# Optimization experiments

Measured on AMD Instinct MI355X. Metric: run time of the kernel, lower is better.

Reference implementation:

```python
import jax, jax.numpy as jnp
import numpy as np

B, T, I, H, O = 64, 512, 256, 512, 1


def _rnn_layer(x, W_ih, W_hh, b_ih, b_hh):
    """One ReLU-RNN layer. x: [B,T,D] -> [B,T,H]."""
    # Precompute input projection for all timesteps as one big GEMM.
    xw = jnp.einsum('btd,hd->bth', x, W_ih) + b_ih + b_hh  # [B,T,H]

    def step(h, xt):
        h = jax.nn.relu(xt + h @ W_hh.T)  # [B,H]
        return h, h

    h0 = jnp.zeros((x.shape[0], W_hh.shape[0]), x.dtype)
    _, out = jax.lax.scan(step, h0, jnp.swapaxes(xw, 0, 1))  # [T,B,H]
    return jnp.swapaxes(out, 0, 1)


def setup_inputs() -> dict:
    key = jax.random.key(0)
    ks = jax.random.split(key, 11)
    s_i = 1.0 / np.sqrt(H)
    inp = {
        'x': jax.random.normal(ks[0], (B, T, I), dtype=jnp.float32),
        'W_ih0': jax.random.uniform(ks[1], (H, I), jnp.float32, -s_i, s_i),
        'W_hh0': jax.random.uniform(ks[2], (H, H), jnp.float32, -s_i, s_i),
        'b_ih0': jax.random.uniform(ks[3], (H,), jnp.float32, -s_i, s_i),
        'b_hh0': jax.random.uniform(ks[4], (H,), jnp.float32, -s_i, s_i),
        'W_ih1': jax.random.uniform(ks[5], (H, H), jnp.float32, -s_i, s_i),
        'W_hh1': jax.random.uniform(ks[6], (H, H), jnp.float32, -s_i, s_i),
        'b_ih1': jax.random.uniform(ks[7], (H,), jnp.float32, -s_i, s_i),
        'b_hh1': jax.random.uniform(ks[8], (H,), jnp.float32, -s_i, s_i),
        'W_fc': jax.random.uniform(ks[9], (O, H), jnp.float32, -s_i, s_i),
        'b_fc': jax.random.uniform(ks[10], (O,), jnp.float32, -s_i, s_i),
    }
    return inp


def reference(x, W_ih0, W_hh0, b_ih0, b_hh0, W_ih1, W_hh1, b_ih1, b_hh1, W_fc, b_fc):
    h = _rnn_layer(x, W_ih0, W_hh0, b_ih0, b_hh0)   # layer 0
    h = _rnn_layer(h, W_ih1, W_hh1, b_ih1, b_hh1)   # layer 1
    logits = jnp.einsum('bth,oh->bto', h, W_fc) + b_fc
    return jax.nn.sigmoid(logits)  # [B,T,O]
```

## Files before the change

### kernel.cpp

```cpp
#include <hip/hip_runtime.h>


typedef _Float16 half8 __attribute__((ext_vector_type(8)));
typedef _Float16 half4 __attribute__((ext_vector_type(4)));
typedef float    f32x4 __attribute__((ext_vector_type(4)));

#define T_DIM 512
#define H_DIM 512
#define B_DIM 64
#define CHUNK 16

#define RAW_BARRIER() asm volatile("s_waitcnt lgkmcnt(0)\n\ts_barrier" ::: "memory")

__global__ __launch_bounds__(256) void conv_w_f16(
    const float* __restrict__ in, _Float16* __restrict__ out)
{
    int i = (blockIdx.x * 256 + threadIdx.x) * 4;
    float4 v = *(const float4*)(in + i);
    out[i + 0] = (_Float16)v.x;
    out[i + 1] = (_Float16)v.y;
    out[i + 2] = (_Float16)v.z;
    out[i + 3] = (_Float16)v.w;
}

__global__ __launch_bounds__(64) void init_flags(int* flags)
{
    flags[threadIdx.x & 31] = 0;
}

__global__ __launch_bounds__(256) void gemm_proj0(
    const float* __restrict__ A32,
    const float* __restrict__ W,
    const float* __restrict__ b1,
    const float* __restrict__ b2,
    _Float16* __restrict__ xwF)
{
    __shared__ float As[16][68];
    __shared__ float Bs[16][68];

    const int tx = threadIdx.x & 15;
    const int ty = threadIdx.x >> 4;
    const int t  = blockIdx.x;
    const int n0 = blockIdx.y * 64;

    float acc[4][4] = {};
    const int rr  = threadIdx.x >> 2;
    const int kk4 = (threadIdx.x & 3) * 4;

    for (int kc = 0; kc < 256; kc += 16) {
        {
            float4 av = *(const float4*)(A32 + (size_t)(rr * T_DIM + t) * 256 + kc + kk4);
            As[kk4 + 0][rr] = av.x; As[kk4 + 1][rr] = av.y;
            As[kk4 + 2][rr] = av.z; As[kk4 + 3][rr] = av.w;
            float4 wv = *(const float4*)(W + (size_t)(n0 + rr) * 256 + kc + kk4);
            Bs[kk4 + 0][rr] = wv.x; Bs[kk4 + 1][rr] = wv.y;
            Bs[kk4 + 2][rr] = wv.z; Bs[kk4 + 3][rr] = wv.w;
        }
        __syncthreads();
#pragma unroll
        for (int kk = 0; kk < 16; ++kk) {
            float4 av = *(const float4*)&As[kk][ty * 4];
            float4 bv = *(const float4*)&Bs[kk][tx * 4];
            float a[4] = {av.x, av.y, av.z, av.w};
            float b[4] = {bv.x, bv.y, bv.z, bv.w};
#pragma unroll
            for (int i = 0; i < 4; ++i)
#pragma unroll
                for (int j = 0; j < 4; ++j)
                    acc[i][j] = fmaf(a[i], b[j], acc[i][j]);
        }
        __syncthreads();
    }

#pragma unroll
    for (int j = 0; j < 4; ++j) {
        int n = n0 + tx * 4 + j;
        float bias = b1[n] + b2[n];
        half4 hv;
#pragma unroll
        for (int i = 0; i < 4; ++i) hv[i] = (_Float16)(acc[i][j] + bias);
        size_t addr = ((size_t)t * 4 + (ty >> 2)) * 8192
                    + ((size_t)blockIdx.y * 4 + (tx >> 2)) * 256
                    + (ty & 3) * 64 + ((tx & 3) * 4 + j) * 4;
        *(half4*)&xwF[addr] = hv;
    }
}

__global__ __launch_bounds__(512, 2) void pipeline(
    const _Float16* __restrict__ xwF0,
    _Float16* __restrict__ xwF1,
    _Float16* __restrict__ h0A,
    const _Float16* __restrict__ W16_0,
    const _Float16* __restrict__ W16_1,
    const float* __restrict__ Wih1,
    const float* __restrict__ bih1,
    const float* __restrict__ bhh1,
    const float* __restrict__ wfc,
    float* __restrict__ part,
    int* __restrict__ flags)
{
    __shared__ _Float16 smem[65536];

    const int bx   = blockIdx.x;
    const int tid  = threadIdx.x;
    const int w    = tid >> 6;
    const int lane = tid & 63;
    const int col  = lane & 15;
    const int q    = lane >> 4;

    int* flag0 = flags;
    int* flag1 = flags + 4;

    if (bx >= 4 && bx < 20) {
        const int g = (bx - 4) >> 2;
        const int s = (bx - 4) & 3;
        _Float16* Bls = smem;

        for (int grp = w; grp < 128; grp += 8) {
            int kt = grp >> 3, nt = grp & 7;
            int n  = s * 128 + nt * 16 + col;
            int k0 = kt * 32 + q * 8;
            float4 a = *(const float4*)(Wih1 + (size_t)n * 512 + k0);
            float4 b = *(const float4*)(Wih1 + (size_t)n * 512 + k0 + 4);
            half8 hv;
            hv[0] = (_Float16)a.x; hv[1] = (_Float16)a.y;
            hv[2] = (_Float16)a.z; hv[3] = (_Float16)a.w;
            hv[4] = (_Float16)b.x; hv[5] = (_Float16)b.y;
            hv[6] = (_Float16)b.z; hv[7] = (_Float16)b.w;
            *(half8*)&Bls[(grp * 64 + lane) * 8] = hv;
        }
        float bias[8];
#pragma unroll
        for (int nt = 0; nt < 8; ++nt) {
            int n = s * 128 + nt * 16 + col;
            bias[nt] = bih1[n] + bhh1[n];
        }
        __syncthreads();

        for (int c = 0; c < T_DIM / CHUNK; ++c) {
            while (__hip_atomic_load(&flag0[g], __ATOMIC_ACQUIRE,
                                     __HIP_MEMORY_SCOPE_AGENT) < c + 1)
                __builtin_amdgcn_s_sleep(2);

#pragma unroll
            for (int i = 0; i < 2; ++i) {
                int t = c * CHUNK + w * 2 + i;
                f32x4 acc[8] = {};
#pragma unroll
                for (int kt = 0; kt < 16; ++kt) {
                    half8 a = *(const half8*)(
                        h0A + ((size_t)(g * T_DIM + t) * 16 + kt) * 512 + lane * 8);
#pragma unroll
                    for (int nt = 0; nt < 8; ++nt) {
                        half8 bfr = *(const half8*)&Bls[((kt * 8 + nt) * 64 + lane) * 8];
                        acc[nt] = __builtin_amdgcn_mfma_f32_16x16x32_f16(
                            a, bfr, acc[nt], 0, 0, 0);
                    }
                }
                _Float16* dst = xwF1 + ((size_t)t * 4 + g) * 8192;
#pragma unroll
                for (int nt = 0; nt < 8; ++nt) {
                    half4 hv;
#pragma unroll
                    for (int r = 0; r < 4; ++r)
                        hv[r] = (_Float16)(acc[nt][r] + bias[nt]);
                    *(half4*)(dst + (s * 8 + nt) * 256 + q * 64 + col * 4) = hv;
                }
            }
            __syncthreads();
            if (tid == 0)
                __hip_atomic_store(&flag1[g * 4 + s], c + 1, __ATOMIC_RELEASE,
                                   __HIP_MEMORY_SCOPE_AGENT);
        }
        return;
    }

    const bool L0 = (bx < 4);
    const int  g  = L0 ? bx : bx - 20;
    const _Float16* W16 = L0 ? W16_0 : W16_1;
    const _Float16* xwF = L0 ? xwF0 : xwF1;

    _Float16* WlB = smem;
    _Float16* hA  = smem + 49152;

    {
        half8 z = {};
        half8* p = (half8*)hA;
        for (int i = tid; i < 1024; i += 512) p[i] = z;
    }
#pragma unroll
    for (int kt = 0; kt < 3; ++kt)
#pragma unroll
        for (int nt = 0; nt < 4; ++nt)
            *(half8*)&WlB[((kt * 32 + w * 4 + nt) * 512) + lane * 8] =
                *(const half8*)(W16 + (size_t)(w * 64 + nt * 16 + col) * 512
                                + (13 + kt) * 32 + q * 8);
    half8 wreg[13][4];
#pragma unroll
    for (int kt = 0; kt < 13; ++kt)
#pragma unroll
        for (int nt = 0; nt < 4; ++nt)
            wreg[kt][nt] = *(const half8*)(
                W16 + (size_t)(w * 64 + nt * 16 + col) * 512 + kt * 32 + q * 8);

    float wfn[4] = {};
    if (!L0) {
#pragma unroll
        for (int nt = 0; nt < 4; ++nt) wfn[nt] = wfc[w * 64 + nt * 16 + col];
    }

    __syncthreads();

    for (int t = 0; t < T_DIM; ++t) {
        if (!L0 && (t & (CHUNK - 1)) == 0) {
            int need = (t >> 4) + 1;
#pragma unroll
            for (int s4 = 0; s4 < 4; ++s4)
                while (__hip_atomic_load(&flag1[g * 4 + s4], __ATOMIC_ACQUIRE,
                                         __HIP_MEMORY_SCOPE_AGENT) < need)
                    __builtin_amdgcn_s_sleep(2);
        }

        half4 xv[4];
        {
            const _Float16* xwp = xwF + ((size_t)t * 4 + g) * 8192;
#pragma unroll
            for (int nt = 0; nt < 4; ++nt)
                xv[nt] = *(const half4*)(xwp + (w * 4 + nt) * 256 + q * 64 + col * 4);
        }

        f32x4 acc[4] = {};
#pragma unroll
        for (int kt = 0; kt < 16; ++kt) {
            half8 a = *(const half8*)&hA[(kt * 64 + lane) * 8];
#pragma unroll
            for (int nt = 0; nt < 4; ++nt) {
                half8 b;
                if (kt < 13) b = wreg[kt][nt];
                else b = *(const half8*)&WlB[(((kt - 13) * 32 + w * 4 + nt) * 512)
                                             + lane * 8];
                acc[nt] = __builtin_amdgcn_mfma_f32_16x16x32_f16(a, b, acc[nt], 0, 0, 0);
            }
        }
        RAW_BARRIER();

        float v[4][4];
#pragma unroll
        for (int nt = 0; nt < 4; ++nt) {
            int nn = nt * 16 + col;
            int kt_a = 2 * w + (nn >> 5);
            int qa   = (nn >> 3) & 3;
            int jj   = nn & 7;
#pragma unroll
            for (int r = 0; r < 4; ++r) {
                float vv = fmaxf(acc[nt][r] + (float)xv[nt][r], 0.f);
                v[nt][r] = vv;
                hA[(kt_a * 64 + qa * 16 + q * 4 + r) * 8 + jj] = (_Float16)vv;
            }
        }
        RAW_BARRIER();

        if (L0) {
#pragma unroll
            for (int e = 0; e < 2; ++e) {
                half8 hv = *(const half8*)&hA[((w * 2 + e) * 64 + lane) * 8];
                *(half8*)(h0A + ((size_t)(g * T_DIM + t) * 16 + w * 2 + e) * 512
                          + lane * 8) = hv;
            }
            if ((t & (CHUNK - 1)) == CHUNK - 1) {
                __syncthreads();
                if (tid == 0)
                    __hip_atomic_store(&flag0[g], (t >> 4) + 1, __ATOMIC_RELEASE,
                                       __HIP_MEMORY_SCOPE_AGENT);
            }
        } else {
            float p[4];
#pragma unroll
            for (int r = 0; r < 4; ++r) {
                p[r] = v[0][r] * wfn[0] + v[1][r] * wfn[1]
                     + v[2][r] * wfn[2] + v[3][r] * wfn[3];
#pragma unroll
                for (int s = 1; s < 16; s <<= 1) p[r] += __shfl_xor(p[r], s);
            }
            if (col == 0) {
                f32x4 pv = {p[0], p[1], p[2], p[3]};
                *(f32x4*)(part + ((size_t)(w * 4 + g) * T_DIM + t) * 16 + q * 4) = pv;
            }
        }
    }
}

__global__ __launch_bounds__(256) void fc_epilogue(
    const float* __restrict__ part, const float* __restrict__ bfc,
    float* __restrict__ outp)
{
    int i = blockIdx.x * 256 + threadIdx.x;
    int b = i >> 9, t = i & 511;
    int g = b >> 4, m = b & 15;
    float s = bfc[0];
#pragma unroll
    for (int w = 0; w < 8; ++w)
        s += part[((size_t)(w * 4 + g) * T_DIM + t) * 16 + m];
    outp[i] = 1.f / (1.f + __expf(-s));
}

extern "C" void kernel_launch(void* const* d_in, const int* in_sizes, int n_in,
                              void* d_out, int out_size, void* d_ws, size_t ws_size,
                              hipStream_t stream)
{
    const float* x     = (const float*)d_in[0];
    const float* W_ih0 = (const float*)d_in[1];
    const float* W_hh0 = (const float*)d_in[2];
    const float* b_ih0 = (const float*)d_in[3];
    const float* b_hh0 = (const float*)d_in[4];
    const float* W_ih1 = (const float*)d_in[5];
    const float* W_hh1 = (const float*)d_in[6];
    const float* b_ih1 = (const float*)d_in[7];
    const float* b_hh1 = (const float*)d_in[8];
    const float* W_fc  = (const float*)d_in[9];
    const float* b_fc  = (const float*)d_in[10];

    _Float16* xwF0  = (_Float16*)d_ws;
    _Float16* xwF1  = xwF0 + (size_t)T_DIM * 4 * 8192;
    _Float16* h0A   = xwF1 + (size_t)T_DIM * 4 * 8192;
    _Float16* W16_0 = h0A + (size_t)4 * T_DIM * 16 * 512;
    _Float16* W16_1 = W16_0 + (size_t)H_DIM * H_DIM;
    float*    partf = (float*)(W16_1 + (size_t)H_DIM * H_DIM);
    int*      flags = (int*)(partf + (size_t)8 * 4 * T_DIM * 16);

    init_flags<<<1, 64, 0, stream>>>(flags);
    conv_w_f16<<<256, 256, 0, stream>>>(W_hh0, W16_0);
    conv_w_f16<<<256, 256, 0, stream>>>(W_hh1, W16_1);

    gemm_proj0<<<dim3(T_DIM, 8), 256, 0, stream>>>(x, W_ih0, b_ih0, b_hh0, xwF0);

    pipeline<<<24, 512, 0, stream>>>(xwF0, xwF1, h0A, W16_0, W16_1,
                                     W_ih1, b_ih1, b_hh1, W_fc, partf, flags);

    fc_epilogue<<<(B_DIM * T_DIM) / 256, 256, 0, stream>>>(partf, b_fc, (float*)d_out);
}
```

Before: 1.777 ms.

## Fuse layer-0 input projection into pipelined kernel and use 4-wave recurrent blocks

Removes the separate fp32 layer-0 projection GEMM and computes it inside the persistent pipeline kernel with MFMA, using dedicated producer blocks that publish per-chunk flags. The recurrent blocks now wait on those flags instead of having the whole projection finished up front. Recurrent blocks go from 512 to 256 threads, and each wave now owns 128 output columns with 12 k-tiles of weights held in registers. The hidden state moves to a padded row-major LDS buffer. This adds register pressure and changes the grid to 40 blocks. It also lengthens the recurrence per wave, since each wave does twice the MFMAs per step.

```diff
diff --git a/kernel.cpp b/kernel.cpp
--- a/kernel.cpp
+++ b/kernel.cpp
@@ -7,7 +7,6 @@
 
 #define T_DIM 512
 #define H_DIM 512
-#define B_DIM 64
 #define CHUNK 16
 
 #define RAW_BARRIER() asm volatile("s_waitcnt lgkmcnt(0)\n\ts_barrier" ::: "memory")
@@ -25,81 +24,30 @@
 
 __global__ __launch_bounds__(64) void init_flags(int* flags)
 {
-    flags[threadIdx.x & 31] = 0;
-}
-
-__global__ __launch_bounds__(256) void gemm_proj0(
-    const float* __restrict__ A32,
-    const float* __restrict__ W,
-    const float* __restrict__ b1,
-    const float* __restrict__ b2,
-    _Float16* __restrict__ xwF)
-{
-    __shared__ float As[16][68];
-    __shared__ float Bs[16][68];
-
-    const int tx = threadIdx.x & 15;
-    const int ty = threadIdx.x >> 4;
-    const int t  = blockIdx.x;
-    const int n0 = blockIdx.y * 64;
-
-    float acc[4][4] = {};
-    const int rr  = threadIdx.x >> 2;
-    const int kk4 = (threadIdx.x & 3) * 4;
-
-    for (int kc = 0; kc < 256; kc += 16) {
-        {
-            float4 av = *(const float4*)(A32 + (size_t)(rr * T_DIM + t) * 256 + kc + kk4);
-            As[kk4 + 0][rr] = av.x; As[kk4 + 1][rr] = av.y;
-            As[kk4 + 2][rr] = av.z; As[kk4 + 3][rr] = av.w;
-            float4 wv = *(const float4*)(W + (size_t)(n0 + rr) * 256 + kc + kk4);
-            Bs[kk4 + 0][rr] = wv.x; Bs[kk4 + 1][rr] = wv.y;
-            Bs[kk4 + 2][rr] = wv.z; Bs[kk4 + 3][rr] = wv.w;
-        }
-        __syncthreads();
-#pragma unroll
-        for (int kk = 0; kk < 16; ++kk) {
-            float4 av = *(const float4*)&As[kk][ty * 4];
-            float4 bv = *(const float4*)&Bs[kk][tx * 4];
-            float a[4] = {av.x, av.y, av.z, av.w};
-            float b[4] = {bv.x, bv.y, bv.z, bv.w};
-#pragma unroll
-            for (int i = 0; i < 4; ++i)
-#pragma unroll
-                for (int j = 0; j < 4; ++j)
-                    acc[i][j] = fmaf(a[i], b[j], acc[i][j]);
-        }
-        __syncthreads();
-    }
-
-#pragma unroll
-    for (int j = 0; j < 4; ++j) {
-        int n = n0 + tx * 4 + j;
-        float bias = b1[n] + b2[n];
-        half4 hv;
-#pragma unroll
-        for (int i = 0; i < 4; ++i) hv[i] = (_Float16)(acc[i][j] + bias);
-        size_t addr = ((size_t)t * 4 + (ty >> 2)) * 8192
-                    + ((size_t)blockIdx.y * 4 + (tx >> 2)) * 256
-                    + (ty & 3) * 64 + ((tx & 3) * 4 + j) * 4;
-        *(half4*)&xwF[addr] = hv;
-    }
-}
-
-__global__ __launch_bounds__(512, 2) void pipeline(
-    const _Float16* __restrict__ xwF0,
-    _Float16* __restrict__ xwF1,
-    _Float16* __restrict__ h0A,
-    const _Float16* __restrict__ W16_0,
-    const _Float16* __restrict__ W16_1,
+    flags[threadIdx.x] = 0;
+}
+
+#define WSTASH 0
+#define HBUF   65536
+
+__global__ __launch_bounds__(256, 1) void pipeline(
+    const float* __restrict__ x,
+    const float* __restrict__ Wih0,
+    const float* __restrict__ bih0,
+    const float* __restrict__ bhh0,
     const float* __restrict__ Wih1,
     const float* __restrict__ bih1,
     const float* __restrict__ bhh1,
+    const _Float16* __restrict__ W16_0,
+    const _Float16* __restrict__ W16_1,
     const float* __restrict__ wfc,
+    _Float16* __restrict__ xwF0,
+    _Float16* __restrict__ xwF1,
+    _Float16* __restrict__ h0,
     float* __restrict__ part,
     int* __restrict__ flags)
 {
-    __shared__ _Float16 smem[65536];
+    __shared__ _Float16 smem[73856];
 
     const int bx   = blockIdx.x;
     const int tid  = threadIdx.x;
@@ -108,183 +56,243 @@
     const int col  = lane & 15;
     const int q    = lane >> 4;
 
-    int* flag0 = flags;
-    int* flag1 = flags + 4;
-
-    if (bx >= 4 && bx < 20) {
-        const int g = (bx - 4) >> 2;
-        const int s = (bx - 4) & 3;
-        _Float16* Bls = smem;
-
-        for (int grp = w; grp < 128; grp += 8) {
-            int kt = grp >> 3, nt = grp & 7;
-            int n  = s * 128 + nt * 16 + col;
-            int k0 = kt * 32 + q * 8;
-            float4 a = *(const float4*)(Wih1 + (size_t)n * 512 + k0);
-            float4 b = *(const float4*)(Wih1 + (size_t)n * 512 + k0 + 4);
-            half8 hv;
-            hv[0] = (_Float16)a.x; hv[1] = (_Float16)a.y;
-            hv[2] = (_Float16)a.z; hv[3] = (_Float16)a.w;
-            hv[4] = (_Float16)b.x; hv[5] = (_Float16)b.y;
-            hv[6] = (_Float16)b.z; hv[7] = (_Float16)b.w;
-            *(half8*)&Bls[(grp * 64 + lane) * 8] = hv;
-        }
+    int* flag_xw0 = flags;
+    int* flag_h0  = flags + 16;
+    int* flag_xw1 = flags + 20;
+
+    if (bx < 16) {
+        const int g = bx >> 2, s = bx & 3;
+
+        half8 wb[8][8];
         float bias[8];
 #pragma unroll
         for (int nt = 0; nt < 8; ++nt) {
-            int n = s * 128 + nt * 16 + col;
+            int n = w * 128 + nt * 16 + col;
+            bias[nt] = bih0[n] + bhh0[n];
+#pragma unroll
+            for (int kt = 0; kt < 8; ++kt) {
+                const float* p = Wih0 + (size_t)n * 256 + kt * 32 + q * 8;
+                float4 f0 = *(const float4*)p;
+                float4 f1 = *(const float4*)(p + 4);
+                half8 hv;
+                hv[0]=(_Float16)f0.x; hv[1]=(_Float16)f0.y;
+                hv[2]=(_Float16)f0.z; hv[3]=(_Float16)f0.w;
+                hv[4]=(_Float16)f1.x; hv[5]=(_Float16)f1.y;
+                hv[6]=(_Float16)f1.z; hv[7]=(_Float16)f1.w;
+                wb[kt][nt] = hv;
+            }
+        }
+
+        for (int c = 0; c < T_DIM / CHUNK; ++c) {
+#pragma unroll
+            for (int i = 0; i < 4; ++i) {
+                int t = c * CHUNK + s * 4 + i;
+                f32x4 acc[8] = {};
+#pragma unroll
+                for (int kt = 0; kt < 8; ++kt) {
+                    const float* p = x + ((size_t)(g * 16 + col) * T_DIM + t) * 256
+                                       + kt * 32 + q * 8;
+                    float4 a0 = *(const float4*)p;
+                    float4 a1 = *(const float4*)(p + 4);
+                    half8 ah;
+                    ah[0]=(_Float16)a0.x; ah[1]=(_Float16)a0.y;
+                    ah[2]=(_Float16)a0.z; ah[3]=(_Float16)a0.w;
+                    ah[4]=(_Float16)a1.x; ah[5]=(_Float16)a1.y;
+                    ah[6]=(_Float16)a1.z; ah[7]=(_Float16)a1.w;
+#pragma unroll
+                    for (int nt = 0; nt < 8; ++nt)
+                        acc[nt] = __builtin_amdgcn_mfma_f32_16x16x32_f16(
+                            ah, wb[kt][nt], acc[nt], 0, 0, 0);
+                }
+                _Float16* dst = xwF0 + ((size_t)t * 4 + g) * 8192 + lane * 4;
+#pragma unroll
+                for (int nt = 0; nt < 8; ++nt) {
+                    half4 hv;
+#pragma unroll
+                    for (int r = 0; r < 4; ++r)
+                        hv[r] = (_Float16)(acc[nt][r] + bias[nt]);
+                    *(half4*)(dst + (w * 8 + nt) * 256) = hv;
+                }
+            }
+            __syncthreads();
+            if (tid == 0)
+                __hip_atomic_store(&flag_xw0[g * 4 + s], c + 1, __ATOMIC_RELEASE,
+                                   __HIP_MEMORY_SCOPE_AGENT);
+        }
+        return;
+    }
+
+    if (bx < 32) {
+        const int g = (bx - 16) >> 2, s = (bx - 16) & 3;
+
+        half8 wb[12][8];
+        float bias[8];
+#pragma unroll
+        for (int nt = 0; nt < 8; ++nt) {
+            int n = w * 128 + nt * 16 + col;
             bias[nt] = bih1[n] + bhh1[n];
+#pragma unroll
+            for (int kt = 0; kt < 16; ++kt) {
+                const float* p = Wih1 + (size_t)n * 512 + kt * 32 + q * 8;
+                float4 f0 = *(const float4*)p;
+                float4 f1 = *(const float4*)(p + 4);
+                half8 hv;
+                hv[0]=(_Float16)f0.x; hv[1]=(_Float16)f0.y;
+                hv[2]=(_Float16)f0.z; hv[3]=(_Float16)f0.w;
+                hv[4]=(_Float16)f1.x; hv[5]=(_Float16)f1.y;
+                hv[6]=(_Float16)f1.z; hv[7]=(_Float16)f1.w;
+                if (kt < 12) wb[kt][nt] = hv;
+                else *(half8*)&smem[WSTASH + w * 16384
+                                    + (((kt - 12) * 8 + nt) * 64 + lane) * 8] = hv;
+            }
         }
         __syncthreads();
 
         for (int c = 0; c < T_DIM / CHUNK; ++c) {
-            while (__hip_atomic_load(&flag0[g], __ATOMIC_ACQUIRE,
+            while (__hip_atomic_load(&flag_h0[g], __ATOMIC_ACQUIRE,
                                      __HIP_MEMORY_SCOPE_AGENT) < c + 1)
                 __builtin_amdgcn_s_sleep(2);
-
-#pragma unroll
-            for (int i = 0; i < 2; ++i) {
-                int t = c * CHUNK + w * 2 + i;
+#pragma unroll
+            for (int i = 0; i < 4; ++i) {
+                int t = c * CHUNK + s * 4 + i;
                 f32x4 acc[8] = {};
 #pragma unroll
                 for (int kt = 0; kt < 16; ++kt) {
-                    half8 a = *(const half8*)(
-                        h0A + ((size_t)(g * T_DIM + t) * 16 + kt) * 512 + lane * 8);
+                    half8 ah = *(const half8*)(
+                        h0 + ((size_t)(g * T_DIM + t) * 16 + col) * 512
+                           + kt * 32 + q * 8);
 #pragma unroll
                     for (int nt = 0; nt < 8; ++nt) {
-                        half8 bfr = *(const half8*)&Bls[((kt * 8 + nt) * 64 + lane) * 8];
+                        half8 b;
+                        if (kt < 12) b = wb[kt][nt];
+                        else b = *(const half8*)&smem[WSTASH + w * 16384
+                                 + (((kt - 12) * 8 + nt) * 64 + lane) * 8];
                         acc[nt] = __builtin_amdgcn_mfma_f32_16x16x32_f16(
-                            a, bfr, acc[nt], 0, 0, 0);
+                            ah, b, acc[nt], 0, 0, 0);
                     }
                 }
-                _Float16* dst = xwF1 + ((size_t)t * 4 + g) * 8192;
+                _Float16* dst = xwF1 + ((size_t)t * 4 + g) * 8192 + lane * 4;
 #pragma unroll
                 for (int nt = 0; nt < 8; ++nt) {
                     half4 hv;
 #pragma unroll
                     for (int r = 0; r < 4; ++r)
                         hv[r] = (_Float16)(acc[nt][r] + bias[nt]);
-                    *(half4*)(dst + (s * 8 + nt) * 256 + q * 64 + col * 4) = hv;
+                    *(half4*)(dst + (w * 8 + nt) * 256) = hv;
                 }
             }
             __syncthreads();
             if (tid == 0)
-                __hip_atomic_store(&flag1[g * 4 + s], c + 1, __ATOMIC_RELEASE,
+                __hip_atomic_store(&flag_xw1[g * 4 + s], c + 1, __ATOMIC_RELEASE,
                                    __HIP_MEMORY_SCOPE_AGENT);
         }
         return;
     }
 
-    const bool L0 = (bx < 4);
-    const int  g  = L0 ? bx : bx - 20;
+    const bool L0 = (bx < 36);
+    const int  g  = L0 ? bx - 32 : bx - 36;
     const _Float16* W16 = L0 ? W16_0 : W16_1;
     const _Float16* xwF = L0 ? xwF0 : xwF1;
-
-    _Float16* WlB = smem;
-    _Float16* hA  = smem + 49152;
-
-    {
-        half8 z = {};
-        half8* p = (half8*)hA;
-        for (int i = tid; i < 1024; i += 512) p[i] = z;
+    int* waitf = L0 ? flag_xw0 : flag_xw1;
+
+    for (int i = tid; i < 16 * 520; i += 256) smem[HBUF + i] = (_Float16)0.f;
+
+#pragma unroll
+    for (int kt4 = 0; kt4 < 4; ++kt4)
+#pragma unroll
+        for (int nt = 0; nt < 8; ++nt)
+            *(half8*)&smem[WSTASH + w * 16384 + ((kt4 * 8 + nt) * 64 + lane) * 8] =
+                *(const half8*)(W16 + (size_t)(w * 128 + nt * 16 + col) * 512
+                                + (12 + kt4) * 32 + q * 8);
+    half8 wreg[12][8];
+#pragma unroll
+    for (int kt = 0; kt < 12; ++kt)
+#pragma unroll
+        for (int nt = 0; nt < 8; ++nt)
+            wreg[kt][nt] = *(const half8*)(
+                W16 + (size_t)(w * 128 + nt * 16 + col) * 512 + kt * 32 + q * 8);
+
+    float wfn[8] = {};
+    if (!L0) {
+#pragma unroll
+        for (int nt = 0; nt < 8; ++nt) wfn[nt] = wfc[w * 128 + nt * 16 + col];
     }
-#pragma unroll
-    for (int kt = 0; kt < 3; ++kt)
-#pragma unroll
-        for (int nt = 0; nt < 4; ++nt)
-            *(half8*)&WlB[((kt * 32 + w * 4 + nt) * 512) + lane * 8] =
-                *(const half8*)(W16 + (size_t)(w * 64 + nt * 16 + col) * 512
-                                + (13 + kt) * 32 + q * 8);
-    half8 wreg[13][4];
-#pragma unroll
-    for (int kt = 0; kt < 13; ++kt)
-#pragma unroll
-        for (int nt = 0; nt < 4; ++nt)
-            wreg[kt][nt] = *(const half8*)(
-                W16 + (size_t)(w * 64 + nt * 16 + col) * 512 + kt * 32 + q * 8);
-
-    float wfn[4] = {};
-    if (!L0) {
-#pragma unroll
-        for (int nt = 0; nt < 4; ++nt) wfn[nt] = wfc[w * 64 + nt * 16 + col];
-    }
 
     __syncthreads();
 
     for (int t = 0; t < T_DIM; ++t) {
-        if (!L0 && (t & (CHUNK - 1)) == 0) {
+        if ((t & (CHUNK - 1)) == 0) {
             int need = (t >> 4) + 1;
 #pragma unroll
             for (int s4 = 0; s4 < 4; ++s4)
-                while (__hip_atomic_load(&flag1[g * 4 + s4], __ATOMIC_ACQUIRE,
+                while (__hip_atomic_load(&waitf[g * 4 + s4], __ATOMIC_ACQUIRE,
                                          __HIP_MEMORY_SCOPE_AGENT) < need)
                     __builtin_amdgcn_s_sleep(2);
         }
 
-        half4 xv[4];
+        half4 xv[8];
         {
-            const _Float16* xwp = xwF + ((size_t)t * 4 + g) * 8192;
-#pragma unroll
-            for (int nt = 0; nt < 4; ++nt)
-                xv[nt] = *(const half4*)(xwp + (w * 4 + nt) * 256 + q * 64 + col * 4);
-        }
-
-        f32x4 acc[4] = {};
+            const _Float16* xwp = xwF + ((size_t)t * 4 + g) * 8192 + lane * 4;
+#pragma unroll
+            for (int nt = 0; nt < 8; ++nt)
+                xv[nt] = *(const half4*)(xwp + (w * 8 + nt) * 256);
+        }
+
+        f32x4 acc[8] = {};
 #pragma unroll
         for (int kt = 0; kt < 16; ++kt) {
-            half8 a = *(const half8*)&hA[(kt * 64 + lane) * 8];
-#pragma unroll
-            for (int nt = 0; nt < 4; ++nt) {
+            half8 a = *(const half8*)&smem[HBUF + col * 520 + kt * 32 + q * 8];
+#pragma unroll
+            for (int nt = 0; nt < 8; ++nt) {
                 half8 b;
-                if (kt < 13) b = wreg[kt][nt];
-                else b = *(const half8*)&WlB[(((kt - 13) * 32 + w * 4 + nt) * 512)
-                                             + lane * 8];
+                if (kt < 12) b = wreg[kt][nt];
+                else b = *(const half8*)&smem[WSTASH + w * 16384
+                         + (((kt - 12) * 8 + nt) * 64 + lane) * 8];
                 acc[nt] = __builtin_amdgcn_mfma_f32_16x16x32_f16(a, b, acc[nt], 0, 0, 0);
             }
         }
         RAW_BARRIER();
 
-        float v[4][4];
-#pragma unroll
-        for (int nt = 0; nt < 4; ++nt) {
-            int nn = nt * 16 + col;
-            int kt_a = 2 * w + (nn >> 5);
-            int qa   = (nn >> 3) & 3;
-            int jj   = nn & 7;
+        float p0 = 0.f, p1 = 0.f, p2 = 0.f, p3 = 0.f;
+#pragma unroll
+        for (int nt = 0; nt < 8; ++nt) {
+            int n = w * 128 + nt * 16 + col;
 #pragma unroll
             for (int r = 0; r < 4; ++r) {
-                float vv = fmaxf(acc[nt][r] + (float)xv[nt][r], 0.f);
-                v[nt][r] = vv;
-                hA[(kt_a * 64 + qa * 16 + q * 4 + r) * 8 + jj] = (_Float16)vv;
+                float v = fmaxf(acc[nt][r] + (float)xv[nt][r], 0.f);
+                smem[HBUF + (q * 4 + r) * 520 + n] = (_Float16)v;
+                if (!L0) {
+                    float pv = v * wfn[nt];
+                    if (r == 0) p0 += pv; else if (r == 1) p1 += pv;
+                    else if (r == 2) p2 += pv; else p3 += pv;
+                }
             }
         }
         RAW_BARRIER();
 
         if (L0) {
-#pragma unroll
-            for (int e = 0; e < 2; ++e) {
-                half8 hv = *(const half8*)&hA[((w * 2 + e) * 64 + lane) * 8];
-                *(half8*)(h0A + ((size_t)(g * T_DIM + t) * 16 + w * 2 + e) * 512
-                          + lane * 8) = hv;
+            int m = w * 4 + q;
+#pragma unroll
+            for (int seg = 0; seg < 4; ++seg) {
+                half8 hv = *(const half8*)&smem[HBUF + m * 520 + col * 32 + seg * 8];
+                *(half8*)(h0 + ((size_t)(g * T_DIM + t) * 16 + m) * 512
+                          + col * 32 + seg * 8) = hv;
             }
             if ((t & (CHUNK - 1)) == CHUNK - 1) {
                 __syncthreads();
                 if (tid == 0)
-                    __hip_atomic_store(&flag0[g], (t >> 4) + 1, __ATOMIC_RELEASE,
+                    __hip_atomic_store(&flag_h0[g], (t >> 4) + 1, __ATOMIC_RELEASE,
                                        __HIP_MEMORY_SCOPE_AGENT);
             }
         } else {
-            float p[4];
-#pragma unroll
-            for (int r = 0; r < 4; ++r) {
-                p[r] = v[0][r] * wfn[0] + v[1][r] * wfn[1]
-                     + v[2][r] * wfn[2] + v[3][r] * wfn[3];
-#pragma unroll
-                for (int s = 1; s < 16; s <<= 1) p[r] += __shfl_xor(p[r], s);
+#pragma unroll
+            for (int s2 = 1; s2 < 16; s2 <<= 1) {
+                p0 += __shfl_xor(p0, s2); p1 += __shfl_xor(p1, s2);
+                p2 += __shfl_xor(p2, s2); p3 += __shfl_xor(p3, s2);
             }
             if (col == 0) {
-                f32x4 pv = {p[0], p[1], p[2], p[3]};
-                *(f32x4*)(part + ((size_t)(w * 4 + g) * T_DIM + t) * 16 + q * 4) = pv;
+                f32x4 pv = {p0, p1, p2, p3};
+                *(f32x4*)(part + ((size_t)(g * 4 + w) * T_DIM + t) * 16 + q * 4) = pv;
             }
         }
     }
@@ -299,8 +307,8 @@
     int g = b >> 4, m = b & 15;
     float s = bfc[0];
 #pragma unroll
-    for (int w = 0; w < 8; ++w)
-        s += part[((size_t)(w * 4 + g) * T_DIM + t) * 16 + m];
+    for (int w = 0; w < 4; ++w)
+        s += part[((size_t)(g * 4 + w) * T_DIM + t) * 16 + m];
     outp[i] = 1.f / (1.f + __expf(-s));
 }
 
@@ -322,20 +330,20 @@
 
     _Float16* xwF0  = (_Float16*)d_ws;
     _Float16* xwF1  = xwF0 + (size_t)T_DIM * 4 * 8192;
-    _Float16* h0A   = xwF1 + (size_t)T_DIM * 4 * 8192;
-    _Float16* W16_0 = h0A + (size_t)4 * T_DIM * 16 * 512;
+    _Float16* h0    = xwF1 + (size_t)T_DIM * 4 * 8192;
+    _Float16* W16_0 = h0 + (size_t)4 * T_DIM * 16 * 512;
     _Float16* W16_1 = W16_0 + (size_t)H_DIM * H_DIM;
     float*    partf = (float*)(W16_1 + (size_t)H_DIM * H_DIM);
-    int*      flags = (int*)(partf + (size_t)8 * 4 * T_DIM * 16);
+    int*      flags = (int*)(partf + (size_t)16 * T_DIM * 16);
 
     init_flags<<<1, 64, 0, stream>>>(flags);
     conv_w_f16<<<256, 256, 0, stream>>>(W_hh0, W16_0);
     conv_w_f16<<<256, 256, 0, stream>>>(W_hh1, W16_1);
 
-    gemm_proj0<<<dim3(T_DIM, 8), 256, 0, stream>>>(x, W_ih0, b_ih0, b_hh0, xwF0);
-
-    pipeline<<<24, 512, 0, stream>>>(xwF0, xwF1, h0A, W16_0, W16_1,
-                                     W_ih1, b_ih1, b_hh1, W_fc, partf, flags);
-
-    fc_epilogue<<<(B_DIM * T_DIM) / 256, 256, 0, stream>>>(partf, b_fc, (float*)d_out);
-}
+    pipeline<<<40, 256, 0, stream>>>(x, W_ih0, b_ih0, b_hh0,
+                                     W_ih1, b_ih1, b_hh1,
+                                     W16_0, W16_1, W_fc,
+                                     xwF0, xwF1, h0, partf, flags);
+
+    fc_epilogue<<<(64 * T_DIM) / 256, 256, 0, stream>>>(partf, b_fc, (float*)d_out);
+}
```

New measurement: 1.732 ms. 1.03x faster.
